# Optimization experiments

Hardware: AMD Instinct MI355X
Metric: run time of the kernel (lower is better)

Reference implementation:

```python
import jax, jax.numpy as jnp
import numpy as np
import math

B, S, H, D = 4, 2048, 16, 64
HID = H * D  # 1024


def setup_inputs() -> dict:
    key = jax.random.key(0)
    ks = jax.random.split(key, 9)
    s_in = 1.0 / math.sqrt(D)
    s_hid = 1.0 / math.sqrt(HID)
    return {
        "x": jax.random.normal(ks[0], (B, S, D), dtype=jnp.float32),
        "Wq": jax.random.uniform(ks[1], (D, HID), jnp.float32, -s_in, s_in),
        "bq": jax.random.uniform(ks[2], (HID,), jnp.float32, -s_in, s_in),
        "Wk": jax.random.uniform(ks[3], (D, HID), jnp.float32, -s_in, s_in),
        "bk": jax.random.uniform(ks[4], (HID,), jnp.float32, -s_in, s_in),
        "Wv": jax.random.uniform(ks[5], (D, HID), jnp.float32, -s_in, s_in),
        "bv": jax.random.uniform(ks[6], (HID,), jnp.float32, -s_in, s_in),
        "Wo": jax.random.uniform(ks[7], (HID, D), jnp.float32, -s_hid, s_hid),
        "bo": jax.random.uniform(ks[8], (D,), jnp.float32, -s_hid, s_hid),
    }


def reference(x, Wq, bq, Wk, bk, Wv, bv, Wo, bo):
    b, s, _ = x.shape
    # projections: [B,S,D] -> [B,S,HID] -> [B,H,S,D]
    q = (x @ Wq + bq).reshape(b, s, H, D).transpose(0, 2, 1, 3)
    k = (x @ Wk + bk).reshape(b, s, H, D).transpose(0, 2, 1, 3)
    v = (x @ Wv + bv).reshape(b, s, H, D).transpose(0, 2, 1, 3)
    scores = jnp.einsum("bhqd,bhkd->bhqk", q, k) / math.sqrt(D)
    # causal mask: -inf strictly above the diagonal
    causal = jnp.tril(jnp.ones((s, s), dtype=bool))
    scores = jnp.where(causal, scores, -jnp.inf)
    attn = jax.nn.softmax(scores, axis=-1)  # dropout is identity at eval
    out = jnp.einsum("bhqk,bhkd->bhqd", attn, v)
    out = out.transpose(0, 2, 1, 3).reshape(b, s, HID)
    return out @ Wo + bo  # [B,S,D]
```

## Files before the change

kernel.cpp:

```cpp
#include <hip/hip_runtime.h>
#include <hip/hip_bf16.h>

#define B 4
#define S 2048
#define H 16
#define D 64
#define HID 1024

typedef __hip_bfloat16 bf16;
typedef __attribute__((ext_vector_type(8))) short bf16x8;
typedef __attribute__((ext_vector_type(4))) short bf16x4;
typedef __attribute__((ext_vector_type(4))) float f32x4;

static __device__ __forceinline__ float b2f(bf16 v) { return __bfloat162float(v); }

static __device__ __forceinline__ unsigned pkbf(float a, float b) {
    union { bf16 h; unsigned short u; } ua, ub;
    ua.h = __float2bfloat16(a);
    ub.h = __float2bfloat16(b);
    return (unsigned)ua.u | ((unsigned)ub.u << 16);
}

#define SCL 0.18033688011112042f

#define QSTR 72
#define VTS  132

__global__ __launch_bounds__(256) void qkv_mfma_kernel(
    const float* __restrict__ x,
    const float* __restrict__ Wq, const float* __restrict__ bq,
    const float* __restrict__ Wk, const float* __restrict__ bk,
    const float* __restrict__ Wv, const float* __restrict__ bv,
    bf16* __restrict__ q, bf16* __restrict__ k, bf16* __restrict__ v)
{
    __shared__ __align__(16) char smem[36864];
    __shared__ float bs[128];
    bf16* Xs = (bf16*)smem;
    bf16* Wt = (bf16*)(smem + 128 * QSTR * 2);

    const int tid = threadIdx.x;
    const int mat = blockIdx.y >> 3;
    const int N0  = (blockIdx.y & 7) * 128;
    const int m0  = blockIdx.x * 128;

    const float* W    = (mat == 0) ? Wq : (mat == 1) ? Wk : Wv;
    const float* bias = (mat == 0) ? bq : (mat == 1) ? bk : bv;
    bf16*        dst  = (mat == 0) ? q  : (mat == 1) ? k  : v;
    const float  oscale = (mat == 0) ? SCL : 1.0f;

    #pragma unroll
    for (int i = 0; i < 8; ++i) {
        int item = i * 256 + tid;
        int row = item >> 4, f4 = item & 15;
        float4 xv = *(const float4*)&x[(size_t)(m0 + row) * D + f4 * 4];
        union { bf16 h[4]; bf16x4 v4; } u;
        u.h[0] = __float2bfloat16(xv.x); u.h[1] = __float2bfloat16(xv.y);
        u.h[2] = __float2bfloat16(xv.z); u.h[3] = __float2bfloat16(xv.w);
        *(bf16x4*)&Xs[row * QSTR + f4 * 4] = u.v4;
    }
    #pragma unroll
    for (int i = 0; i < 2; ++i) {
        int unit = i * 256 + tid;
        int n0 = (unit & 31) * 4, k0 = (unit >> 5) * 4;
        float wv[4][4];
        #pragma unroll
        for (int j = 0; j < 4; ++j) {
            float4 t = *(const float4*)&W[(size_t)(k0 + j) * HID + N0 + n0];
            wv[j][0] = t.x; wv[j][1] = t.y; wv[j][2] = t.z; wv[j][3] = t.w;
        }
        #pragma unroll
        for (int dn = 0; dn < 4; ++dn) {
            union { bf16 h[4]; bf16x4 v4; } u;
            #pragma unroll
            for (int j = 0; j < 4; ++j) u.h[j] = __float2bfloat16(wv[j][dn]);
            *(bf16x4*)&Wt[(n0 + dn) * QSTR + k0] = u.v4;
        }
    }
    if (tid < 128) bs[tid] = bias[N0 + tid];
    __syncthreads();

    const int lane = tid & 63, wave = tid >> 6;
    const int c = lane & 15, quad = lane >> 4;

    bf16x8 af[2][2];
    #pragma unroll
    for (int mg = 0; mg < 2; ++mg)
        #pragma unroll
        for (int kc = 0; kc < 2; ++kc)
            af[mg][kc] = *(const bf16x8*)&Xs[(wave * 32 + mg * 16 + c) * QSTR + kc * 32 + quad * 8];

    f32x4 acc[2][8];
    #pragma unroll
    for (int mg = 0; mg < 2; ++mg)
        #pragma unroll
        for (int ng = 0; ng < 8; ++ng)
            acc[mg][ng] = (f32x4){0.f, 0.f, 0.f, 0.f};

    const int b_ = m0 >> 11, ss0 = m0 & (S - 1);

    if (mat == 2) {
        #pragma unroll
        for (int ng = 0; ng < 8; ++ng) {
            bf16x8 bf0 = *(const bf16x8*)&Wt[(ng * 16 + c) * QSTR + quad * 8];
            bf16x8 bf1 = *(const bf16x8*)&Wt[(ng * 16 + c) * QSTR + 32 + quad * 8];
            #pragma unroll
            for (int mg = 0; mg < 2; ++mg) {
                acc[mg][ng] = __builtin_amdgcn_mfma_f32_16x16x32_bf16(af[mg][0], bf0, acc[mg][ng], 0, 0, 0);
                acc[mg][ng] = __builtin_amdgcn_mfma_f32_16x16x32_bf16(af[mg][1], bf1, acc[mg][ng], 0, 0, 0);
            }
        }
        bf16* T = (bf16*)smem;
        __syncthreads();
        #pragma unroll
        for (int ng = 0; ng < 8; ++ng) {
            int hid_l = ng * 16 + c;
            float bb_ = bs[hid_l];
            #pragma unroll
            for (int mg = 0; mg < 2; ++mg) {
                int ss_l = wave * 32 + mg * 16 + quad * 4;
                union { bf16 h4[4]; bf16x4 v4; } u;
                #pragma unroll
                for (int r = 0; r < 4; ++r)
                    u.h4[r] = __float2bfloat16(acc[mg][ng][r] + bb_);
                *(bf16x4*)&T[hid_l * VTS + ss_l] = u.v4;
            }
        }
        __syncthreads();
        #pragma unroll
        for (int pass = 0; pass < 8; ++pass) {
            int unit = pass * 256 + tid;
            int dd_l = unit >> 4, u8 = unit & 15;
            bf16x8 val = *(const bf16x8*)&T[dd_l * VTS + u8 * 8];
            int h = (N0 >> 6) + (dd_l >> 6), ddg = dd_l & 63;
            *(bf16x8*)&dst[((size_t)(b_ * H + h) * D + ddg) * S + ss0 + u8 * 8] = val;
        }
    } else {
        #pragma unroll
        for (int ng = 0; ng < 8; ++ng) {
            bf16x8 bf0 = *(const bf16x8*)&Wt[(ng * 16 + c) * QSTR + quad * 8];
            bf16x8 bf1 = *(const bf16x8*)&Wt[(ng * 16 + c) * QSTR + 32 + quad * 8];
            #pragma unroll
            for (int mg = 0; mg < 2; ++mg) {
                acc[mg][ng] = __builtin_amdgcn_mfma_f32_16x16x32_bf16(bf0, af[mg][0], acc[mg][ng], 0, 0, 0);
                acc[mg][ng] = __builtin_amdgcn_mfma_f32_16x16x32_bf16(bf1, af[mg][1], acc[mg][ng], 0, 0, 0);
            }
        }
        #pragma unroll
        for (int ng = 0; ng < 8; ++ng) {
            float4 bb4 = *(const float4*)&bs[ng * 16 + quad * 4];
            int n_g = N0 + ng * 16 + quad * 4;
            int h = n_g >> 6, dd = n_g & 63;
            #pragma unroll
            for (int mg = 0; mg < 2; ++mg) {
                int mrow = wave * 32 + mg * 16 + c;
                union { bf16 h4[4]; bf16x4 v4; } u;
                #pragma unroll
                for (int r = 0; r < 4; ++r)
                    u.h4[r] = __float2bfloat16((acc[mg][ng][r] + (&bb4.x)[r]) * oscale);
                *(bf16x4*)&dst[((size_t)(b_ * H + h) * S + ss0 + mrow) * D + dd] = u.v4;
            }
        }
    }
}

#define BT   64
#define NT   (S / BT)

__global__ __launch_bounds__(256) void flash_mfma_kernel(
    const bf16* __restrict__ qg, const bf16* __restrict__ kg,
    const bf16* __restrict__ vg, bf16* __restrict__ og)
{
    __shared__ bf16 Ks[2][BT * 64];
    __shared__ bf16 Vt[2][BT * 64];
    __shared__ bf16 Ps[4][16 * 64];

    const int tid  = threadIdx.x;
    const int wave = tid >> 6;
    const int lane = tid & 63;
    const int c    = lane & 15;
    const int quad = lane >> 4;

    const int L    = (int)blockIdx.x + 16 * (int)blockIdx.y;
    const int xcd  = L & 7;
    const int slot = L >> 3;
    const int pair = slot & 15;
    const int bh   = xcd * 8 + (slot >> 4);
    const int b_   = bh >> 4, h_ = bh & 15;
    const size_t hbase = (size_t)bh * S * D;
    bf16* myP = &Ps[wave][0];
    const int srow = wave * 16 + c;

    const int qta = pair;
    const int qtb = NT - 1 - pair;

    const int cx7 = c & 7;

    const int rA = wave * 16 + (lane >> 3);
    const int rB = rA + 8;
    const int gA = (((lane & 7) ^ (rA & 7)) << 3);

    auto gld = [](const bf16* g, bf16* l) {
        __builtin_amdgcn_global_load_lds(
            (const __attribute__((address_space(1))) void*)g,
            (__attribute__((address_space(3))) void*)l, 16, 0, 0);
    };
    auto stageTile = [&](int buf, int nb) {
        bf16* kb = &Ks[buf][wave * 1024];
        bf16* vb = &Vt[buf][wave * 1024];
        gld(kg + hbase + (size_t)(nb + rA) * D + gA, kb);
        gld(kg + hbase + (size_t)(nb + rB) * D + gA, kb + 512);
        gld(vg + hbase + (size_t)rA * S + nb + gA, vb);
        gld(vg + hbase + (size_t)rB * S + nb + gA, vb + 512);
    };

    bf16x8 qfa0, qfa1, qfb0, qfb1;
    {
        const size_t ra = hbase + (size_t)(qta * BT + srow) * D;
        const size_t rb = hbase + (size_t)(qtb * BT + srow) * D;
        qfa0 = *(const bf16x8*)(qg + ra + quad * 8);
        qfa1 = *(const bf16x8*)(qg + ra + 32 + quad * 8);
        qfb0 = *(const bf16x8*)(qg + rb + quad * 8);
        qfb1 = *(const bf16x8*)(qg + rb + 32 + quad * 8);
    }

    float la = 0.f, lb = 0.f;
    f32x4 ota[4], otb[4];
    #pragma unroll
    for (int jn = 0; jn < 4; ++jn) {
        ota[jn] = (f32x4){0.f, 0.f, 0.f, 0.f};
        otb[jn] = (f32x4){0.f, 0.f, 0.f, 0.f};
    }

    auto front = [&](const bf16* Kb, bf16x8 qf0, bf16x8 qf1, float& l1, bool diag) {
        f32x4 st[4];
        #pragma unroll
        for (int jn = 0; jn < 4; ++jn) {
            const int rb_ = (jn * 16 + c) * 64;
            bf16x8 kf0 = *(const bf16x8*)&Kb[rb_ + ((quad       ^ cx7) << 3)];
            bf16x8 kf1 = *(const bf16x8*)&Kb[rb_ + (((quad + 4) ^ cx7) << 3)];
            f32x4 s = {0.f, 0.f, 0.f, 0.f};
            s = __builtin_amdgcn_mfma_f32_16x16x32_bf16(kf0, qf0, s, 0, 0, 0);
            s = __builtin_amdgcn_mfma_f32_16x16x32_bf16(kf1, qf1, s, 0, 0, 0);
            st[jn] = s;
        }
        #pragma unroll
        for (int jn = 0; jn < 4; ++jn) {
            float p0 = __builtin_amdgcn_exp2f(st[jn][0]);
            float p1 = __builtin_amdgcn_exp2f(st[jn][1]);
            float p2 = __builtin_amdgcn_exp2f(st[jn][2]);
            float p3 = __builtin_amdgcn_exp2f(st[jn][3]);
            if (diag) {
                int col = jn * 16 + quad * 4;
                if (col     > srow) p0 = 0.f;
                if (col + 1 > srow) p1 = 0.f;
                if (col + 2 > srow) p2 = 0.f;
                if (col + 3 > srow) p3 = 0.f;
            }
            l1 += (p0 + p1) + (p2 + p3);
            uint2 pk;
            pk.x = pkbf(p0, p1);
            pk.y = pkbf(p2, p3);
            *(uint2*)&myP[c * 64 + (((2 * jn + (quad >> 1)) ^ cx7) << 3) + (quad & 1) * 4] = pk;
        }
    };
    auto pv = [&](const bf16* Vb, f32x4* ot) {
        #pragma unroll
        for (int kc = 0; kc < 2; ++kc) {
            bf16x8 pf = *(const bf16x8*)&myP[c * 64 + (((kc * 4 + quad) ^ cx7) << 3)];
            #pragma unroll
            for (int jn = 0; jn < 4; ++jn) {
                const int rb_ = (jn * 16 + c) * 64;
                bf16x8 vf = *(const bf16x8*)&Vb[rb_ + (((kc * 4 + quad) ^ cx7) << 3)];
                ot[jn] = __builtin_amdgcn_mfma_f32_16x16x32_bf16(vf, pf, ot[jn], 0, 0, 0);
            }
        }
    };

    stageTile(0, 0);
    __syncthreads();

    int cur = 0;
    for (int kt = 0; kt <= qtb; ++kt) {
        if (kt < qtb) stageTile(cur ^ 1, (kt + 1) * BT);

        const bf16* Kb = &Ks[cur][0];
        const bf16* Vb = &Vt[cur][0];
        front(Kb, qfb0, qfb1, lb, kt == qtb);
        asm volatile("s_waitcnt lgkmcnt(0)" ::: "memory");
        pv(Vb, otb);
        if (kt <= qta) {
            front(Kb, qfa0, qfa1, la, kt == qta);
            asm volatile("s_waitcnt lgkmcnt(0)" ::: "memory");
            pv(Vb, ota);
        }

        if (kt < qtb) {
            __syncthreads();
            cur ^= 1;
        }
    }

    {
        float lt = lb;
        lt += __shfl_xor(lt, 16);
        lt += __shfl_xor(lt, 32);
        const float inv = 1.f / lt;
        const size_t obase = ((size_t)(b_ * S + qtb * BT + srow)) * HID + h_ * 64 + quad * 4;
        #pragma unroll
        for (int jn = 0; jn < 4; ++jn) {
            union { bf16 h4[4]; bf16x4 v4; } u;
            #pragma unroll
            for (int r = 0; r < 4; ++r)
                u.h4[r] = __float2bfloat16(otb[jn][r] * inv);
            *(bf16x4*)&og[obase + jn * 16] = u.v4;
        }
    }
    {
        float lt = la;
        lt += __shfl_xor(lt, 16);
        lt += __shfl_xor(lt, 32);
        const float inv = 1.f / lt;
        const size_t obase = ((size_t)(b_ * S + qta * BT + srow)) * HID + h_ * 64 + quad * 4;
        #pragma unroll
        for (int jn = 0; jn < 4; ++jn) {
            union { bf16 h4[4]; bf16x4 v4; } u;
            #pragma unroll
            for (int r = 0; r < 4; ++r)
                u.h4[r] = __float2bfloat16(ota[jn][r] * inv);
            *(bf16x4*)&og[obase + jn * 16] = u.v4;
        }
    }
}

__global__ __launch_bounds__(256) void out_proj_mfma_kernel(
    const bf16* __restrict__ o, const float* __restrict__ Wo,
    const float* __restrict__ bo, float* __restrict__ out)
{
    __shared__ bf16 Os[2][32 * QSTR];
    __shared__ bf16 Wot[2][64 * QSTR];
    __shared__ float bos[64];

    const int tid = threadIdx.x;
    const int m0  = blockIdx.x * 32;
    const int lane = tid & 63, wave = tid >> 6;
    const int c = lane & 15, quad = lane >> 4;
    const int mtile = wave >> 1;
    const int ngb   = (wave & 1) * 2;

    const int orow = tid >> 3, ooct = tid & 7;
    const int n0 = (tid & 15) * 4, kk0 = (tid >> 4) * 4;

    if (tid < 64) bos[tid] = bo[tid];

    bf16x8 oreg = *(const bf16x8*)(o + (size_t)(m0 + orow) * HID + ooct * 8);
    float4 w4[4];
    #pragma unroll
    for (int j = 0; j < 4; ++j)
        w4[j] = *(const float4*)&Wo[(size_t)(kk0 + j) * 64 + n0];

    auto stage = [&](int buf) {
        *(bf16x8*)&Os[buf][orow * QSTR + ooct * 8] = oreg;
        #pragma unroll
        for (int dn = 0; dn < 4; ++dn) {
            union { bf16 h[4]; bf16x4 v4; } u;
            u.h[0] = __float2bfloat16((&w4[0].x)[dn]);
            u.h[1] = __float2bfloat16((&w4[1].x)[dn]);
            u.h[2] = __float2bfloat16((&w4[2].x)[dn]);
            u.h[3] = __float2bfloat16((&w4[3].x)[dn]);
            *(bf16x4*)&Wot[buf][(n0 + dn) * QSTR + kk0] = u.v4;
        }
    };

    stage(0);
    {
        const int k1 = 64;
        oreg = *(const bf16x8*)(o + (size_t)(m0 + orow) * HID + k1 + ooct * 8);
        #pragma unroll
        for (int j = 0; j < 4; ++j)
            w4[j] = *(const float4*)&Wo[(size_t)(k1 + kk0 + j) * 64 + n0];
    }
    __syncthreads();

    f32x4 acc[2];
    acc[0] = (f32x4){0.f, 0.f, 0.f, 0.f};
    acc[1] = (f32x4){0.f, 0.f, 0.f, 0.f};

    int cur = 0;
    for (int chunk = 0; chunk < 16; ++chunk) {
        if (chunk < 15) {
            stage(cur ^ 1);
            if (chunk + 1 < 15) {
                const int k2 = (chunk + 2) * 64;
                oreg = *(const bf16x8*)(o + (size_t)(m0 + orow) * HID + k2 + ooct * 8);
                #pragma unroll
                for (int j = 0; j < 4; ++j)
                    w4[j] = *(const float4*)&Wo[(size_t)(k2 + kk0 + j) * 64 + n0];
            }
        }

        bf16x8 a0 = *(const bf16x8*)&Os[cur][(mtile * 16 + c) * QSTR + quad * 8];
        bf16x8 a1 = *(const bf16x8*)&Os[cur][(mtile * 16 + c) * QSTR + 32 + quad * 8];
        #pragma unroll
        for (int g = 0; g < 2; ++g) {
            int ng = ngb + g;
            bf16x8 b0 = *(const bf16x8*)&Wot[cur][(ng * 16 + c) * QSTR + quad * 8];
            bf16x8 b1 = *(const bf16x8*)&Wot[cur][(ng * 16 + c) * QSTR + 32 + quad * 8];
            acc[g] = __builtin_amdgcn_mfma_f32_16x16x32_bf16(a0, b0, acc[g], 0, 0, 0);
            acc[g] = __builtin_amdgcn_mfma_f32_16x16x32_bf16(a1, b1, acc[g], 0, 0, 0);
        }

        if (chunk < 15) {
            __syncthreads();
            cur ^= 1;
        }
    }

    #pragma unroll
    for (int g = 0; g < 2; ++g) {
        int n = (ngb + g) * 16 + c;
        float bb_ = bos[n];
        #pragma unroll
        for (int r = 0; r < 4; ++r) {
            int row = m0 + mtile * 16 + quad * 4 + r;
            out[(size_t)row * 64 + n] = acc[g][r] + bb_;
        }
    }
}

extern "C" void kernel_launch(void* const* d_in, const int* in_sizes, int n_in,
                              void* d_out, int out_size, void* d_ws, size_t ws_size,
                              hipStream_t stream)
{
    const float* x  = (const float*)d_in[0];
    const float* Wq = (const float*)d_in[1];
    const float* bq = (const float*)d_in[2];
    const float* Wk = (const float*)d_in[3];
    const float* bk = (const float*)d_in[4];
    const float* Wv = (const float*)d_in[5];
    const float* bv = (const float*)d_in[6];
    const float* Wo = (const float*)d_in[7];
    const float* bo = (const float*)d_in[8];

    char* ws = (char*)d_ws;
    const size_t qkv_bytes = (size_t)B * S * HID * sizeof(bf16);
    bf16* qw = (bf16*)(ws);
    bf16* kw = (bf16*)(ws + qkv_bytes);
    bf16* vw = (bf16*)(ws + 2 * qkv_bytes);
    bf16* ow = (bf16*)(ws + 3 * qkv_bytes);

    qkv_mfma_kernel<<<dim3(B * S / 128, 24), 256, 0, stream>>>(
        x, Wq, bq, Wk, bk, Wv, bv, qw, kw, vw);

    flash_mfma_kernel<<<dim3(NT / 2, B * H), 256, 0, stream>>>(qw, kw, vw, ow);

    out_proj_mfma_kernel<<<dim3(B * S / 32), 256, 0, stream>>>(ow, Wo, bo,
                                                               (float*)d_out);
}
```

Before: 172.7 us.

## Merge two query-tile pairs per 512-thread block sharing K/V staging

Result: faster. 154.7 us, median of 3 (-10.4%).

```diff
diff --git a/kernel.cpp b/kernel.cpp
--- a/kernel.cpp
+++ b/kernel.cpp
@@ -166,52 +166,40 @@
 #define BT   64
 #define NT   (S / BT)
 
-__global__ __launch_bounds__(256) void flash_mfma_kernel(
+__global__ __launch_bounds__(512) void flash_mfma_kernel(
     const bf16* __restrict__ qg, const bf16* __restrict__ kg,
     const bf16* __restrict__ vg, bf16* __restrict__ og)
 {
     __shared__ bf16 Ks[2][BT * 64];
     __shared__ bf16 Vt[2][BT * 64];
-    __shared__ bf16 Ps[4][16 * 64];
+    __shared__ bf16 Ps[8][16 * 64];
 
     const int tid  = threadIdx.x;
     const int wave = tid >> 6;
     const int lane = tid & 63;
     const int c    = lane & 15;
     const int quad = lane >> 4;
-
-    const int L    = (int)blockIdx.x + 16 * (int)blockIdx.y;
+    const int wg   = wave >> 2;
+    const int wl   = wave & 3;
+
+    const int L    = (int)blockIdx.x + 8 * (int)blockIdx.y;
     const int xcd  = L & 7;
     const int slot = L >> 3;
-    const int pair = slot & 15;
-    const int bh   = xcd * 8 + (slot >> 4);
+    const int u    = slot & 7;
+    const int bh   = xcd * 8 + (slot >> 3);
     const int b_   = bh >> 4, h_ = bh & 15;
     const size_t hbase = (size_t)bh * S * D;
     bf16* myP = &Ps[wave][0];
-    const int srow = wave * 16 + c;
-
-    const int qta = pair;
-    const int qtb = NT - 1 - pair;
-
+    const int srow = wl * 16 + c;
+
+    const int qta    = 2 * u + wg;
+    const int qtb    = 31 - 2 * u - wg;
+    const int qtbmax = 31 - 2 * u;
+
+    const int sr = tid >> 3, g0 = tid & 7;
+    const int sc0 = g0 * 8;
+    const int so  = sr * 64 + ((g0 ^ (sr & 7)) << 3);
     const int cx7 = c & 7;
-
-    const int rA = wave * 16 + (lane >> 3);
-    const int rB = rA + 8;
-    const int gA = (((lane & 7) ^ (rA & 7)) << 3);
-
-    auto gld = [](const bf16* g, bf16* l) {
-        __builtin_amdgcn_global_load_lds(
-            (const __attribute__((address_space(1))) void*)g,
-            (__attribute__((address_space(3))) void*)l, 16, 0, 0);
-    };
-    auto stageTile = [&](int buf, int nb) {
-        bf16* kb = &Ks[buf][wave * 1024];
-        bf16* vb = &Vt[buf][wave * 1024];
-        gld(kg + hbase + (size_t)(nb + rA) * D + gA, kb);
-        gld(kg + hbase + (size_t)(nb + rB) * D + gA, kb + 512);
-        gld(vg + hbase + (size_t)rA * S + nb + gA, vb);
-        gld(vg + hbase + (size_t)rB * S + nb + gA, vb + 512);
-    };
 
     bf16x8 qfa0, qfa1, qfb0, qfb1;
     {
@@ -276,25 +264,44 @@
         }
     };
 
-    stageTile(0, 0);
+    bf16x8 kreg, vreg;
+    kreg = *(const bf16x8*)(kg + hbase + (size_t)sr * D + sc0);
+    vreg = *(const bf16x8*)(vg + hbase + (size_t)sr * S + sc0);
+    *(bf16x8*)&Ks[0][so] = kreg;
+    *(bf16x8*)&Vt[0][so] = vreg;
+    {
+        const int nb = BT;
+        kreg = *(const bf16x8*)(kg + hbase + (size_t)(nb + sr) * D + sc0);
+        vreg = *(const bf16x8*)(vg + hbase + (size_t)sr * S + nb + sc0);
+    }
     __syncthreads();
 
     int cur = 0;
-    for (int kt = 0; kt <= qtb; ++kt) {
-        if (kt < qtb) stageTile(cur ^ 1, (kt + 1) * BT);
+    for (int kt = 0; kt <= qtbmax; ++kt) {
+        if (kt < qtbmax) {
+            *(bf16x8*)&Ks[cur ^ 1][so] = kreg;
+            *(bf16x8*)&Vt[cur ^ 1][so] = vreg;
+            if (kt + 1 < qtbmax) {
+                const int nb = (kt + 2) * BT;
+                kreg = *(const bf16x8*)(kg + hbase + (size_t)(nb + sr) * D + sc0);
+                vreg = *(const bf16x8*)(vg + hbase + (size_t)sr * S + nb + sc0);
+            }
+        }
 
         const bf16* Kb = &Ks[cur][0];
         const bf16* Vb = &Vt[cur][0];
-        front(Kb, qfb0, qfb1, lb, kt == qtb);
-        asm volatile("s_waitcnt lgkmcnt(0)" ::: "memory");
-        pv(Vb, otb);
+        if (kt <= qtb) {
+            front(Kb, qfb0, qfb1, lb, kt == qtb);
+            asm volatile("s_waitcnt lgkmcnt(0)" ::: "memory");
+            pv(Vb, otb);
+        }
         if (kt <= qta) {
             front(Kb, qfa0, qfa1, la, kt == qta);
             asm volatile("s_waitcnt lgkmcnt(0)" ::: "memory");
             pv(Vb, ota);
         }
 
-        if (kt < qtb) {
+        if (kt < qtbmax) {
             __syncthreads();
             cur ^= 1;
         }
@@ -451,7 +458,7 @@
     qkv_mfma_kernel<<<dim3(B * S / 128, 24), 256, 0, stream>>>(
         x, Wq, bq, Wk, bk, Wv, bv, qw, kw, vw);
 
-    flash_mfma_kernel<<<dim3(NT / 2, B * H), 256, 0, stream>>>(qw, kw, vw, ow);
+    flash_mfma_kernel<<<dim3(8, B * H), 512, 0, stream>>>(qw, kw, vw, ow);
 
     out_proj_mfma_kernel<<<dim3(B * S / 32), 256, 0, stream>>>(ow, Wo, bo,
                                                                (float*)d_out);
```
